# Performance work log

Measured on AMD Instinct MI355X. Metric: run time of the kernel, lower is better.

## Reference

```python
import jax, jax.numpy as jnp
import numpy as np

N_NODES = 20000; N_EDGES = 320000; B = 128; T = 200
EMB = 128; GH = 64; HEADS = 4; LH = 128; NSP = 64; TD = 4

def gat_conv(x, src, dst, W, att_src, att_dst, bias, heads, ch, concat):
    # PyG GATConv (eval mode, dropout off): per-edge attention + segment softmax over dst
    n = x.shape[0]
    h = (x @ W).reshape(n, heads, ch)                      # [N,H,C]
    a_s = (h * att_src[None]).sum(-1)                      # [N,H]
    a_d = (h * att_dst[None]).sum(-1)
    e = jax.nn.leaky_relu(a_s[src] + a_d[dst], 0.2)        # [E,H]
    e_max = jax.ops.segment_max(e, dst, num_segments=n)    # every node has a self-loop -> finite
    ex = jnp.exp(e - e_max[dst])
    denom = jax.ops.segment_sum(ex, dst, num_segments=n)
    alpha = ex / denom[dst]                                # [E,H]
    out = jax.ops.segment_sum(h[src] * alpha[:, :, None], dst, num_segments=n)  # [N,H,C]
    out = out.reshape(n, heads * ch) if concat else out.mean(axis=1)
    return out + bias

def lstm_dir(x, w_ih, w_hh, b):
    # single-direction LSTM, torch gate order (i, f, g, o)
    bsz = x.shape[0]
    def step(carry, xt):
        hprev, cprev = carry
        g = xt @ w_ih.T + hprev @ w_hh.T + b
        i, f, gg, o = jnp.split(g, 4, axis=-1)
        c = jax.nn.sigmoid(f) * cprev + jax.nn.sigmoid(i) * jnp.tanh(gg)
        hnew = jax.nn.sigmoid(o) * jnp.tanh(c)
        return (hnew, c), hnew
    init = (jnp.zeros((bsz, LH), x.dtype), jnp.zeros((bsz, LH), x.dtype))
    _, hs = jax.lax.scan(step, init, jnp.swapaxes(x, 0, 1))
    return jnp.swapaxes(hs, 0, 1)

def forward(x_coords, temporal_features, node_emb,
            gat1_W, gat1_att_src, gat1_att_dst, gat1_bias,
            gat2_W, gat2_att_src, gat2_att_dst, gat2_bias,
            w_ih_f, w_hh_f, b_f, w_ih_b, w_hh_b, b_b,
            attn_node_w, attn_node_b, attn_sp_w, attn_sp_b,
            fc_node_W, fc_node_b, fc_sp_W, fc_sp_b,
            edge_index, seq, lengths):
    n = x_coords.shape[0]
    node_features = jnp.concatenate([x_coords, node_emb, temporal_features], axis=1)  # [N,134]
    loops = jnp.arange(n)                                  # PyG GATConv add_self_loops=True
    src = jnp.concatenate([edge_index[0], loops])
    dst = jnp.concatenate([edge_index[1], loops])
    z = jax.nn.elu(gat_conv(node_features, src, dst, gat1_W, gat1_att_src, gat1_att_dst, gat1_bias, HEADS, GH, True))
    z = gat_conv(z, src, dst, gat2_W, gat2_att_src, gat2_att_dst, gat2_bias, 1, EMB, False)
    seq_emb = z[seq]                                       # [B,T,EMB]
    out_f = lstm_dir(seq_emb, w_ih_f, w_hh_f, b_f)
    # backward direction of packed BiLSTM: reverse each sequence within its true length
    rev_idx = jnp.clip(lengths[:, None] - 1 - jnp.arange(T)[None, :], 0, T - 1)
    x_rev = jnp.take_along_axis(seq_emb, rev_idx[:, :, None], axis=1)
    out_b = jnp.take_along_axis(lstm_dir(x_rev, w_ih_b, w_hh_b, b_b), rev_idx[:, :, None], axis=1)
    lstm_out = jnp.concatenate([out_f, out_b], axis=-1)    # [B,T,2*LH]
    mask = jnp.arange(T)[None, :] < lengths[:, None]
    def attnpool(w, bias):
        scores = jnp.where(mask, lstm_out @ w + bias, -jnp.inf)
        aw = jax.nn.softmax(scores, axis=1)
        return jnp.einsum('bt,bth->bh', aw, lstm_out)
    ctx_n = attnpool(attn_node_w, attn_node_b)
    ctx_s = attnpool(attn_sp_w, attn_sp_b)
    return (ctx_n @ fc_node_W + fc_node_b, ctx_s @ fc_sp_W + fc_sp_b)

def setup_inputs() -> dict:
    key = jax.random.key(0)
    ks = jax.random.split(key, 24)
    f = lambda i, shape, s=0.05: jax.random.normal(ks[i], shape, jnp.float32) * s
    return dict(
        x_coords=f(0, (N_NODES, 2), 1.0),
        temporal_features=f(1, (N_NODES, TD), 1.0),
        node_emb=f(2, (N_NODES, EMB)),
        gat1_W=f(3, (2 + EMB + TD, HEADS * GH)),
        gat1_att_src=f(4, (HEADS, GH)),
        gat1_att_dst=f(5, (HEADS, GH)),
        gat1_bias=jnp.zeros((HEADS * GH,), jnp.float32),
        gat2_W=f(6, (HEADS * GH, EMB)),
        gat2_att_src=f(7, (1, EMB)),
        gat2_att_dst=f(8, (1, EMB)),
        gat2_bias=jnp.zeros((EMB,), jnp.float32),
        w_ih_f=f(9, (4 * LH, EMB)), w_hh_f=f(10, (4 * LH, LH)), b_f=jnp.zeros((4 * LH,), jnp.float32),
        w_ih_b=f(11, (4 * LH, EMB)), w_hh_b=f(12, (4 * LH, LH)), b_b=jnp.zeros((4 * LH,), jnp.float32),
        attn_node_w=f(13, (2 * LH,)), attn_node_b=jnp.zeros((1,), jnp.float32),
        attn_sp_w=f(14, (2 * LH,)), attn_sp_b=jnp.zeros((1,), jnp.float32),
        fc_node_W=f(15, (2 * LH, N_NODES)), fc_node_b=jnp.zeros((N_NODES,), jnp.float32),
        fc_sp_W=f(16, (2 * LH, NSP)), fc_sp_b=jnp.zeros((NSP,), jnp.float32),
        edge_index=jax.random.randint(ks[17], (2, N_EDGES), 0, N_NODES),
        seq=jax.random.randint(ks[18], (B, T), 0, N_NODES),
        lengths=jax.random.randint(ks[19], (B,), 1, T + 1),
    )

def reference(x_coords, temporal_features, node_emb,
              gat1_W, gat1_att_src, gat1_att_dst, gat1_bias,
              gat2_W, gat2_att_src, gat2_att_dst, gat2_bias,
              w_ih_f, w_hh_f, b_f, w_ih_b, w_hh_b, b_b,
              attn_node_w, attn_node_b, attn_sp_w, attn_sp_b,
              fc_node_W, fc_node_b, fc_sp_W, fc_sp_b,
              edge_index, seq, lengths):
    return forward(x_coords, temporal_features, node_emb,
                   gat1_W, gat1_att_src, gat1_att_dst, gat1_bias,
                   gat2_W, gat2_att_src, gat2_att_dst, gat2_bias,
                   w_ih_f, w_hh_f, b_f, w_ih_b, w_hh_b, b_b,
                   attn_node_w, attn_node_b, attn_sp_w, attn_sp_b,
                   fc_node_W, fc_node_b, fc_sp_W, fc_sp_b,
                   edge_index, seq, lengths)
```

## Files before the change

kernel.cpp:

```cpp
#include <hip/hip_runtime.h>
#include <cstdint>
#include <cstddef>

#define N_NODES 20000
#define N_EDGES 320000
#define NE_TOT  (N_EDGES + N_NODES)
#define BB 128
#define TT 200
#define EMB 128
#define GH 64
#define HEADS 4
#define LH 128
#define NSP 64
#define KF 136

#define NB_COUNT  ((NE_TOT + 255) / 256)
#define NB_PREP1  (N_NODES + KF)
#define NB_PREP2  ((2 * 512 * 128 + 512 + 255) / 256)
#define NB_ROWMAP ((BB * TT + 255) / 256)

__global__ void k_prep_all(const int* __restrict__ ei, int* __restrict__ cnt,
                           const float* __restrict__ xc, const float* __restrict__ tf,
                           const float* __restrict__ ne, const float* __restrict__ W1,
                           float* __restrict__ nf, float* __restrict__ Wp,
                           const float* __restrict__ wf, const float* __restrict__ wb,
                           const float* __restrict__ bf, const float* __restrict__ bb,
                           float* __restrict__ WT, float* __restrict__ bcat,
                           const int* __restrict__ lengths, const int* __restrict__ seq,
                           int* __restrict__ rowsrc, int* __restrict__ rowdst,
                           int* __restrict__ loff)
{
    int blk = blockIdx.x;
    int tid = threadIdx.x;
    if (blk < NB_COUNT) {
        int e = blk * 256 + tid;
        if (e >= NE_TOT) return;
        int d = (e < N_EDGES) ? ei[N_EDGES + e] : (e - N_EDGES);
        atomicAdd(&cnt[d], 1);
    } else if (blk < NB_COUNT + NB_PREP1) {
        int b2 = blk - NB_COUNT;
        if (b2 < N_NODES) {
            int n = b2, j = tid;
            if (j >= KF) return;
            float v = 0.f;
            if (j < 2)        v = xc[n * 2 + j];
            else if (j < 130) v = ne[n * 128 + (j - 2)];
            else if (j < 134) v = tf[n * 4 + (j - 130)];
            nf[(size_t)n * KF + j] = v;
        } else {
            int k = b2 - N_NODES, n = tid;
            Wp[k * 256 + n] = (k < 134) ? W1[k * 256 + n] : 0.f;
        }
    } else if (blk < NB_COUNT + NB_PREP1 + NB_PREP2) {
        int idx = (blk - NB_COUNT - NB_PREP1) * 256 + tid;
        if (idx < 512 * 128) {
            int g = idx & 511, k = idx >> 9;
            WT[k * 1024 + g] = wf[g * 128 + k];
        } else if (idx < 2 * 512 * 128) {
            int j = idx - 512 * 128;
            int g = j & 511, k = j >> 9;
            WT[k * 1024 + 512 + g] = wb[g * 128 + k];
        } else if (idx < 2 * 512 * 128 + 512) {
            int t = idx - 2 * 512 * 128;
            bcat[t] = bf[t];
            bcat[512 + t] = bb[t];
        }
    } else {
        int idx = (blk - NB_COUNT - NB_PREP1 - NB_PREP2) * 256 + tid;
        if (idx >= BB * TT) return;
        int b = idx / TT, t = idx - b * TT;
        int base = 0;
        for (int i = 0; i < BB; i++) base += (i < b) ? lengths[i] : 0;
        if (idx == 0) {
            int tot = 0;
            for (int i = 0; i < BB; i++) tot += lengths[i];
            loff[BB] = tot;
        }
        if (t >= lengths[b]) return;
        int pos = base + t;
        rowsrc[pos] = seq[idx];
        rowdst[pos] = idx;
    }
}

__global__ __launch_bounds__(1024) void k_scan(const int* __restrict__ cnt,
                                               int* __restrict__ rs,
                                               int* __restrict__ cursor) {
    __shared__ int sd[1024];
    int tid = threadIdx.x;
    const int EPT = 20;
    int base = tid * EPT;
    int v[EPT];
    int s = 0;
#pragma unroll
    for (int i = 0; i < EPT; i++) {
        int idx = base + i;
        v[i] = (idx < N_NODES) ? cnt[idx] : 0;
        s += v[i];
    }
    int x = s;
    sd[tid] = x;
    __syncthreads();
    for (int off = 1; off < 1024; off <<= 1) {
        int t = (tid >= off) ? sd[tid - off] : 0;
        __syncthreads();
        x += t; sd[tid] = x;
        __syncthreads();
    }
    int run = x - s;
#pragma unroll
    for (int i = 0; i < EPT; i++) {
        int idx = base + i;
        if (idx < N_NODES) { rs[idx] = run; cursor[idx] = run; }
        run += v[i];
    }
    if (tid == 1023) rs[N_NODES] = x;
}

__global__ void k_scatter(const int* __restrict__ ei, int* __restrict__ cursor, int* __restrict__ csr) {
    int e = blockIdx.x * blockDim.x + threadIdx.x;
    if (e >= NE_TOT) return;
    int s, d;
    if (e < N_EDGES) { s = ei[e]; d = ei[N_EDGES + e]; }
    else             { s = d = e - N_EDGES; }
    int pos = atomicAdd(&cursor[d], 1);
    csr[pos] = s;
}

__global__ __launch_bounds__(256) void k_gemm_f32(
    const float* __restrict__ A, const float* __restrict__ B, float* __restrict__ C,
    int M, int N, int K, const int* __restrict__ gather, const float* __restrict__ bias,
    const float* __restrict__ asrc, const float* __restrict__ adst,
    float* __restrict__ a_s, float* __restrict__ a_d, int AC)
{
    __shared__ float As[8][68];
    __shared__ float Bs[8][68];
    int tid = threadIdx.x;
    int bm = blockIdx.y << 6, bn = blockIdx.x << 6;
    int tm = (tid >> 4) << 2, tn = (tid & 15) << 2;
    float acc[4][4] = {};
    for (int k0 = 0; k0 < K; k0 += 8) {
        if (tid < 128) {
            int m = tid >> 1, kq = (tid & 1) << 2;
            int gm = bm + m;
            float4 v = make_float4(0.f, 0.f, 0.f, 0.f);
            if (gm < M) {
                int row = gather ? gather[gm] : gm;
                v = *(const float4*)(A + (size_t)row * K + k0 + kq);
            }
            As[kq + 0][m] = v.x; As[kq + 1][m] = v.y;
            As[kq + 2][m] = v.z; As[kq + 3][m] = v.w;
        } else {
            int t2 = tid - 128;
            int kk = t2 >> 4, n4 = (t2 & 15) << 2;
            int gn = bn + n4;
            float4 v = make_float4(0.f, 0.f, 0.f, 0.f);
            const float* brow = B + (size_t)(k0 + kk) * N;
            if (gn + 3 < N) v = *(const float4*)(brow + gn);
            else {
                if (gn + 0 < N) v.x = brow[gn + 0];
                if (gn + 1 < N) v.y = brow[gn + 1];
                if (gn + 2 < N) v.z = brow[gn + 2];
                if (gn + 3 < N) v.w = brow[gn + 3];
            }
            *(float4*)(&Bs[kk][n4]) = v;
        }
        __syncthreads();
#pragma unroll
        for (int k = 0; k < 8; k++) {
            float4 av = *(const float4*)&As[k][tm];
            float4 bv = *(const float4*)&Bs[k][tn];
            acc[0][0] += av.x * bv.x; acc[0][1] += av.x * bv.y; acc[0][2] += av.x * bv.z; acc[0][3] += av.x * bv.w;
            acc[1][0] += av.y * bv.x; acc[1][1] += av.y * bv.y; acc[1][2] += av.y * bv.z; acc[1][3] += av.y * bv.w;
            acc[2][0] += av.z * bv.x; acc[2][1] += av.z * bv.y; acc[2][2] += av.z * bv.z; acc[2][3] += av.z * bv.w;
            acc[3][0] += av.w * bv.x; acc[3][1] += av.w * bv.y; acc[3][2] += av.w * bv.z; acc[3][3] += av.w * bv.w;
        }
        __syncthreads();
    }
#pragma unroll
    for (int i = 0; i < 4; i++) {
        int gm = bm + tm + i;
        if (gm >= M) continue;
#pragma unroll
        for (int j = 0; j < 4; j++) {
            int gn = bn + tn + j;
            if (gn >= N) continue;
            float r = acc[i][j];
            if (bias) r += bias[gn];
            C[(size_t)gm * N + gn] = r;
        }
    }
    if (asrc) {
        int H = N / AC;
        int h = bn / AC;
#pragma unroll
        for (int i = 0; i < 4; i++) {
            int gm = bm + tm + i;
            float ps = 0.f, pd = 0.f;
#pragma unroll
            for (int j = 0; j < 4; j++) {
                int gn = bn + tn + j;
                ps += acc[i][j] * asrc[gn];
                pd += acc[i][j] * adst[gn];
            }
            for (int off = 8; off >= 1; off >>= 1) {
                ps += __shfl_down(ps, off);
                pd += __shfl_down(pd, off);
            }
            if ((tid & 15) == 0 && gm < M) {
                atomicAdd(&a_s[gm * H + h], ps);
                atomicAdd(&a_d[gm * H + h], pd);
            }
        }
    }
}

__global__ __launch_bounds__(256) void k_gemm_f32_rs(
    const float* __restrict__ A, const float* __restrict__ B, float* __restrict__ C,
    const int* __restrict__ Mdev, int N, int K,
    const int* __restrict__ rowsrc, const int* __restrict__ rowdst,
    const float* __restrict__ bias)
{
    int M = Mdev[BB];
    int bm = blockIdx.y << 6, bn = blockIdx.x << 6;
    if (bm >= M) return;
    __shared__ float As[8][68];
    __shared__ float Bs[8][68];
    int tid = threadIdx.x;
    int tm = (tid >> 4) << 2, tn = (tid & 15) << 2;
    float acc[4][4] = {};
    for (int k0 = 0; k0 < K; k0 += 8) {
        if (tid < 128) {
            int m = tid >> 1, kq = (tid & 1) << 2;
            int gm = bm + m;
            float4 v = make_float4(0.f, 0.f, 0.f, 0.f);
            if (gm < M) {
                int row = rowsrc[gm];
                v = *(const float4*)(A + (size_t)row * K + k0 + kq);
            }
            As[kq + 0][m] = v.x; As[kq + 1][m] = v.y;
            As[kq + 2][m] = v.z; As[kq + 3][m] = v.w;
        } else {
            int t2 = tid - 128;
            int kk = t2 >> 4, n4 = (t2 & 15) << 2;
            int gn = bn + n4;
            const float* brow = B + (size_t)(k0 + kk) * N;
            *(float4*)(&Bs[kk][n4]) = *(const float4*)(brow + gn);
        }
        __syncthreads();
#pragma unroll
        for (int k = 0; k < 8; k++) {
            float4 av = *(const float4*)&As[k][tm];
            float4 bv = *(const float4*)&Bs[k][tn];
            acc[0][0] += av.x * bv.x; acc[0][1] += av.x * bv.y; acc[0][2] += av.x * bv.z; acc[0][3] += av.x * bv.w;
            acc[1][0] += av.y * bv.x; acc[1][1] += av.y * bv.y; acc[1][2] += av.y * bv.z; acc[1][3] += av.y * bv.w;
            acc[2][0] += av.z * bv.x; acc[2][1] += av.z * bv.y; acc[2][2] += av.z * bv.z; acc[2][3] += av.z * bv.w;
            acc[3][0] += av.w * bv.x; acc[3][1] += av.w * bv.y; acc[3][2] += av.w * bv.z; acc[3][3] += av.w * bv.w;
        }
        __syncthreads();
    }
#pragma unroll
    for (int i = 0; i < 4; i++) {
        int gm = bm + tm + i;
        if (gm >= M) continue;
        size_t crow = (size_t)rowdst[gm] * N;
#pragma unroll
        for (int j = 0; j < 4; j++) {
            int gn = bn + tn + j;
            float r = acc[i][j] + bias[gn];
            C[crow + gn] = r;
        }
    }
}

__global__ __launch_bounds__(256) void k_gemm_heads(
    const float* __restrict__ ctxn, const float* __restrict__ ctxs,
    const float* __restrict__ Wn, const float* __restrict__ bnod,
    const float* __restrict__ Wsp, const float* __restrict__ bsp,
    float* __restrict__ outn, float* __restrict__ outs)
{
    const float* A; const float* B; float* C; const float* bias; int N; int bn;
    if (blockIdx.x < 313) { A = ctxn; B = Wn;  C = outn; bias = bnod; N = N_NODES; bn = blockIdx.x << 6; }
    else                  { A = ctxs; B = Wsp; C = outs; bias = bsp;  N = NSP;     bn = 0; }
    const int M = BB, K = 2 * LH;
    __shared__ float As[8][68];
    __shared__ float Bs[8][68];
    int tid = threadIdx.x;
    int bm = blockIdx.y << 6;
    int tm = (tid >> 4) << 2, tn = (tid & 15) << 2;
    float acc[4][4] = {};
    for (int k0 = 0; k0 < K; k0 += 8) {
        if (tid < 128) {
            int m = tid >> 1, kq = (tid & 1) << 2;
            int gm = bm + m;
            float4 v = make_float4(0.f, 0.f, 0.f, 0.f);
            if (gm < M) v = *(const float4*)(A + (size_t)gm * K + k0 + kq);
            As[kq + 0][m] = v.x; As[kq + 1][m] = v.y;
            As[kq + 2][m] = v.z; As[kq + 3][m] = v.w;
        } else {
            int t2 = tid - 128;
            int kk = t2 >> 4, n4 = (t2 & 15) << 2;
            int gn = bn + n4;
            float4 v = make_float4(0.f, 0.f, 0.f, 0.f);
            const float* brow = B + (size_t)(k0 + kk) * N;
            if (gn + 3 < N) v = *(const float4*)(brow + gn);
            else {
                if (gn + 0 < N) v.x = brow[gn + 0];
                if (gn + 1 < N) v.y = brow[gn + 1];
                if (gn + 2 < N) v.z = brow[gn + 2];
                if (gn + 3 < N) v.w = brow[gn + 3];
            }
            *(float4*)(&Bs[kk][n4]) = v;
        }
        __syncthreads();
#pragma unroll
        for (int k = 0; k < 8; k++) {
            float4 av = *(const float4*)&As[k][tm];
            float4 bv = *(const float4*)&Bs[k][tn];
            acc[0][0] += av.x * bv.x; acc[0][1] += av.x * bv.y; acc[0][2] += av.x * bv.z; acc[0][3] += av.x * bv.w;
            acc[1][0] += av.y * bv.x; acc[1][1] += av.y * bv.y; acc[1][2] += av.y * bv.z; acc[1][3] += av.y * bv.w;
            acc[2][0] += av.z * bv.x; acc[2][1] += av.z * bv.y; acc[2][2] += av.z * bv.z; acc[2][3] += av.z * bv.w;
            acc[3][0] += av.w * bv.x; acc[3][1] += av.w * bv.y; acc[3][2] += av.w * bv.z; acc[3][3] += av.w * bv.w;
        }
        __syncthreads();
    }
#pragma unroll
    for (int i = 0; i < 4; i++) {
        int gm = bm + tm + i;
        if (gm >= M) continue;
#pragma unroll
        for (int j = 0; j < 4; j++) {
            int gn = bn + tn + j;
            if (gn >= N) continue;
            C[(size_t)gm * N + gn] = acc[i][j] + bias[gn];
        }
    }
}

template <int H, int C, bool DO_ELU>
__global__ void k_gat_aggregate(const float* __restrict__ hm, const float* __restrict__ a_s,
                                const float* __restrict__ a_d, const int* __restrict__ rs,
                                const int* __restrict__ csr, const float* __restrict__ bias,
                                float* __restrict__ out) {
    int d = blockIdx.x;
    int tid = threadIdx.x;
    int h = tid / C;
    int r0 = rs[d], r1 = rs[d + 1];
    float adv = a_d[d * H + h];
    float den = 0.f, acc = 0.f;
    for (int j = r0; j < r1; j++) {
        int s = csr[j];
        float e = a_s[s * H + h] + adv;
        e = (e > 0.f) ? e : 0.2f * e;
        float ex = __expf(e);
        den += ex;
        acc += ex * hm[(size_t)s * (H * C) + tid];
    }
    float r = acc / den + bias[tid];
    if (DO_ELU) r = (r > 0.f) ? r : expm1f(r);
    out[(size_t)d * (H * C) + tid] = r;
}

__device__ __forceinline__ float sigmf(float x) { return 1.f / (1.f + __expf(-x)); }
__device__ __forceinline__ float tanhfast(float x) {
    x = fminf(fmaxf(x, -20.f), 20.f);
    float e = __expf(2.f * x);
    return (e - 1.f) / (e + 1.f);
}

__global__ __launch_bounds__(512, 2) void k_lstm(
    const float* __restrict__ xgcat,
    const float* __restrict__ whh_f, const float* __restrict__ whh_b,
    const int* __restrict__ lengths, float* __restrict__ lstm_out)
{
    int b = blockIdx.x & 127;
    int dir = blockIdx.x >> 7;
    int tid = threadIdx.x;
    int u = tid & 127;
    int j = tid >> 7;
    const float* whh = dir ? whh_b : whh_f;
    const float* xg = xgcat + (dir << 9);
    int L = lengths[b];
    float4 w4[4][8];
#pragma unroll
    for (int m = 0; m < 4; m++) {
        const float4* wrow = (const float4*)(whh + (size_t)(m * LH + u) * LH + j * 32);
#pragma unroll
        for (int q = 0; q < 8; q++) w4[m][q] = wrow[q];
    }
    __shared__ float hbuf[LH];
    __shared__ float pbuf[4][4 * LH];
    if (tid < LH) hbuf[tid] = 0.f;
    float c = 0.f;
    float hv = 0.f;
    float x0 = 0.f, x1 = 0.f, x2 = 0.f, x3 = 0.f;
    if (j == 0) {
        int tx0 = dir ? (L - 1) : 0;
        const float* xrow = xg + ((size_t)(b * TT + tx0) << 10);
        x0 = xrow[u]; x1 = xrow[LH + u]; x2 = xrow[2 * LH + u]; x3 = xrow[3 * LH + u];
    }
    __syncthreads();
    for (int t = 0; t < L; t++) {
        if (j == 0 && t > 0) {
            int txp = dir ? (L - t) : (t - 1);
            lstm_out[((size_t)b * TT + txp) * (2 * LH) + dir * LH + u] = hv;
        }
        float x0n = 0.f, x1n = 0.f, x2n = 0.f, x3n = 0.f;
        if (j == 0 && t + 1 < L) {
            int tx1 = dir ? (L - 2 - t) : (t + 1);
            const float* xrow = xg + ((size_t)(b * TT + tx1) << 10);
            x0n = xrow[u]; x1n = xrow[LH + u]; x2n = xrow[2 * LH + u]; x3n = xrow[3 * LH + u];
        }
        const float4* hp = (const float4*)(hbuf + j * 32);
        float4 h[8];
#pragma unroll
        for (int q = 0; q < 8; q++) h[q] = hp[q];
        float a0 = x0, a1 = x1, a2 = x2, a3 = x3;
#pragma unroll
        for (int q = 0; q < 8; q++) {
            float4 hq = h[q];
            a0 += w4[0][q].x * hq.x + w4[0][q].y * hq.y + w4[0][q].z * hq.z + w4[0][q].w * hq.w;
            a1 += w4[1][q].x * hq.x + w4[1][q].y * hq.y + w4[1][q].z * hq.z + w4[1][q].w * hq.w;
            a2 += w4[2][q].x * hq.x + w4[2][q].y * hq.y + w4[2][q].z * hq.z + w4[2][q].w * hq.w;
            a3 += w4[3][q].x * hq.x + w4[3][q].y * hq.y + w4[3][q].z * hq.z + w4[3][q].w * hq.w;
        }
        pbuf[j][0 * LH + u] = a0;
        pbuf[j][1 * LH + u] = a1;
        pbuf[j][2 * LH + u] = a2;
        pbuf[j][3 * LH + u] = a3;
        asm volatile("s_waitcnt lgkmcnt(0)" ::: "memory");
        __builtin_amdgcn_sched_barrier(0);
        __builtin_amdgcn_s_barrier();
        if (tid < LH) {
            float gi = (pbuf[0][0 * LH + u] + pbuf[1][0 * LH + u]) + (pbuf[2][0 * LH + u] + pbuf[3][0 * LH + u]);
            float gf = (pbuf[0][1 * LH + u] + pbuf[1][1 * LH + u]) + (pbuf[2][1 * LH + u] + pbuf[3][1 * LH + u]);
            float gG = (pbuf[0][2 * LH + u] + pbuf[1][2 * LH + u]) + (pbuf[2][2 * LH + u] + pbuf[3][2 * LH + u]);
            float go = (pbuf[0][3 * LH + u] + pbuf[1][3 * LH + u]) + (pbuf[2][3 * LH + u] + pbuf[3][3 * LH + u]);
            float ig = sigmf(gi);
            float fg = sigmf(gf);
            float gg = tanhfast(gG);
            float og = sigmf(go);
            c = fg * c + ig * gg;
            hv = og * tanhfast(c);
            hbuf[u] = hv;
        }
        asm volatile("s_waitcnt lgkmcnt(0)" ::: "memory");
        __builtin_amdgcn_sched_barrier(0);
        __builtin_amdgcn_s_barrier();
        x0 = x0n; x1 = x1n; x2 = x2n; x3 = x3n;
    }
    if (j == 0) {
        int txp = dir ? 0 : (L - 1);
        lstm_out[((size_t)b * TT + txp) * (2 * LH) + dir * LH + u] = hv;
    }
}

__global__ __launch_bounds__(256) void k_attnpool(
    const float* __restrict__ lo, const int* __restrict__ lengths,
    const float* __restrict__ wn, const float* __restrict__ bn,
    const float* __restrict__ wsp, const float* __restrict__ bsp,
    float* __restrict__ ctxn, float* __restrict__ ctxs)
{
    int b = blockIdx.x;
    int tid = threadIdx.x;
    int L = lengths[b];
    __shared__ float sn[TT], ss[TT];
    __shared__ float red[256];
    int wv = tid >> 6, lane = tid & 63;
    for (int t = wv; t < L; t += 4) {
        const float* row = lo + ((size_t)b * TT + t) * (2 * LH);
        float pn = 0.f, ps = 0.f;
#pragma unroll
        for (int c0 = 0; c0 < 256; c0 += 64) {
            float v = row[c0 + lane];
            pn += v * wn[c0 + lane];
            ps += v * wsp[c0 + lane];
        }
#pragma unroll
        for (int off = 32; off > 0; off >>= 1) {
            pn += __shfl_down(pn, off);
            ps += __shfl_down(ps, off);
        }
        if (lane == 0) { sn[t] = pn + bn[0]; ss[t] = ps + bsp[0]; }
    }
    __syncthreads();
    float vn = (tid < L) ? sn[tid] : -1e30f;
    float vs = (tid < L) ? ss[tid] : -1e30f;
    red[tid] = vn; __syncthreads();
    for (int s = 128; s > 0; s >>= 1) { if (tid < s) red[tid] = fmaxf(red[tid], red[tid + s]); __syncthreads(); }
    float mn = red[0]; __syncthreads();
    red[tid] = vs; __syncthreads();
    for (int s = 128; s > 0; s >>= 1) { if (tid < s) red[tid] = fmaxf(red[tid], red[tid + s]); __syncthreads(); }
    float ms = red[0]; __syncthreads();
    float en = (tid < L) ? __expf(vn - mn) : 0.f;
    float es = (tid < L) ? __expf(vs - ms) : 0.f;
    red[tid] = en; __syncthreads();
    for (int s = 128; s > 0; s >>= 1) { if (tid < s) red[tid] += red[tid + s]; __syncthreads(); }
    float dn = red[0]; __syncthreads();
    red[tid] = es; __syncthreads();
    for (int s = 128; s > 0; s >>= 1) { if (tid < s) red[tid] += red[tid + s]; __syncthreads(); }
    float dsum = red[0]; __syncthreads();
    if (tid < L) { sn[tid] = en / dn; ss[tid] = es / dsum; }
    __syncthreads();
    float an = 0.f, asv = 0.f;
    for (int t = 0; t < L; t++) {
        float v = lo[((size_t)b * TT + t) * (2 * LH) + tid];
        an += sn[t] * v;
        asv += ss[t] * v;
    }
    ctxn[b * (2 * LH) + tid] = an;
    ctxs[b * (2 * LH) + tid] = asv;
}

extern "C" void kernel_launch(void* const* d_in, const int* in_sizes, int n_in,
                              void* d_out, int out_size, void* d_ws, size_t ws_size,
                              hipStream_t stream) {
    (void)in_sizes; (void)n_in; (void)out_size; (void)ws_size;
    const float* x_coords = (const float*)d_in[0];
    const float* temporal = (const float*)d_in[1];
    const float* node_emb = (const float*)d_in[2];
    const float* gat1_W   = (const float*)d_in[3];
    const float* gat1_as  = (const float*)d_in[4];
    const float* gat1_ad  = (const float*)d_in[5];
    const float* gat1_b   = (const float*)d_in[6];
    const float* gat2_W   = (const float*)d_in[7];
    const float* gat2_as  = (const float*)d_in[8];
    const float* gat2_ad  = (const float*)d_in[9];
    const float* gat2_b   = (const float*)d_in[10];
    const float* w_ih_f   = (const float*)d_in[11];
    const float* w_hh_f   = (const float*)d_in[12];
    const float* b_f      = (const float*)d_in[13];
    const float* w_ih_b   = (const float*)d_in[14];
    const float* w_hh_b   = (const float*)d_in[15];
    const float* b_b      = (const float*)d_in[16];
    const float* attn_n_w = (const float*)d_in[17];
    const float* attn_n_b = (const float*)d_in[18];
    const float* attn_s_w = (const float*)d_in[19];
    const float* attn_s_b = (const float*)d_in[20];
    const float* fc_n_W   = (const float*)d_in[21];
    const float* fc_n_b   = (const float*)d_in[22];
    const float* fc_s_W   = (const float*)d_in[23];
    const float* fc_s_b   = (const float*)d_in[24];
    const int*   edge_idx = (const int*)d_in[25];
    const int*   seq      = (const int*)d_in[26];
    const int*   lengths  = (const int*)d_in[27];

    char* ws = (char*)d_ws;
    size_t off = 0;
    auto alloc = [&](size_t bytes) -> char* {
        char* p = ws + off;
        off += (bytes + 255) & ~(size_t)255;
        return p;
    };
    int*   cnt      = (int*)alloc((size_t)N_NODES * 4);
    float* as1      = (float*)alloc((size_t)N_NODES * 4 * 4);
    float* ad1      = (float*)alloc((size_t)N_NODES * 4 * 4);
    float* as2      = (float*)alloc((size_t)N_NODES * 4);
    float* ad2      = (float*)alloc((size_t)N_NODES * 4);
    size_t zero_end = off;
    int*   rowstart = (int*)alloc((size_t)(N_NODES + 1) * 4);
    int*   cursor   = (int*)alloc((size_t)N_NODES * 4);
    int*   csr      = (int*)alloc((size_t)NE_TOT * 4);
    float* z2       = (float*)alloc((size_t)N_NODES * EMB * 4);
    float* lstm_o   = (float*)alloc((size_t)BB * TT * 2 * LH * 4);
    float* ctxn     = (float*)alloc((size_t)BB * 2 * LH * 4);
    float* ctxs     = (float*)alloc((size_t)BB * 2 * LH * 4);
    float* wTcat    = (float*)alloc((size_t)128 * 1024 * 4);
    float* bcat     = (float*)alloc((size_t)1024 * 4);
    int*   loff     = (int*)alloc((size_t)(BB + 1) * 4);
    int*   rowsrc   = (int*)alloc((size_t)BB * TT * 4);
    int*   rowdst   = (int*)alloc((size_t)BB * TT * 4);
    float* nf  = (float*)(ws + off);
    float* w1p = nf + (size_t)N_NODES * KF;
    float* h1  = w1p + (size_t)KF * 256;
    float* z1  = h1 + (size_t)N_NODES * 256;
    float* h2  = z1 + (size_t)N_NODES * 256;
    float* xgcat = (float*)(ws + off);

    hipMemsetAsync(cnt, 0, zero_end, stream);
    k_prep_all<<<NB_COUNT + NB_PREP1 + NB_PREP2 + NB_ROWMAP, 256, 0, stream>>>(
        edge_idx, cnt, x_coords, temporal, node_emb, gat1_W, nf, w1p,
        w_ih_f, w_ih_b, b_f, b_b, wTcat, bcat, lengths, seq, rowsrc, rowdst, loff);
    k_scan<<<1, 1024, 0, stream>>>(cnt, rowstart, cursor);
    k_scatter<<<(NE_TOT + 255) / 256, 256, 0, stream>>>(edge_idx, cursor, csr);
    {
        dim3 g(4, (N_NODES + 63) / 64);
        k_gemm_f32<<<g, 256, 0, stream>>>(nf, w1p, h1, N_NODES, 256, KF, nullptr, nullptr,
                                          gat1_as, gat1_ad, as1, ad1, GH);
    }
    k_gat_aggregate<HEADS, GH, true><<<N_NODES, 256, 0, stream>>>(h1, as1, ad1, rowstart, csr, gat1_b, z1);
    {
        dim3 g(2, (N_NODES + 63) / 64);
        k_gemm_f32<<<g, 256, 0, stream>>>(z1, gat2_W, h2, N_NODES, 128, 256, nullptr, nullptr,
                                          gat2_as, gat2_ad, as2, ad2, EMB);
    }
    k_gat_aggregate<1, EMB, false><<<N_NODES, 128, 0, stream>>>(h2, as2, ad2, rowstart, csr, gat2_b, z2);
    {
        dim3 g(1024 / 64, (BB * TT + 63) / 64);
        k_gemm_f32_rs<<<g, 256, 0, stream>>>(z2, wTcat, xgcat, loff, 1024, 128, rowsrc, rowdst, bcat);
    }
    k_lstm<<<256, 512, 0, stream>>>(xgcat, w_hh_f, w_hh_b, lengths, lstm_o);
    k_attnpool<<<BB, 256, 0, stream>>>(lstm_o, lengths, attn_n_w, attn_n_b, attn_s_w, attn_s_b, ctxn, ctxs);
    float* out_node = (float*)d_out;
    float* out_sp   = out_node + (size_t)BB * N_NODES;
    {
        dim3 g(314, 2);
        k_gemm_heads<<<g, 256, 0, stream>>>(ctxn, ctxs, fc_n_W, fc_n_b, fc_s_W, fc_s_b, out_node, out_sp);
    }
}
```

Before: 687.2 us.

## Rewrite FP32 GEMMs as single-wave 8x8 register tiles with double-buffered LDS

All four dense GEMM kernels (both GAT projections, the LSTM input projection and the output heads) move from 256-thread blocks computing 4x4 per thread to 64-thread single-wavefront blocks computing 8x8 per thread. The next K-slice is prefetched into registers and written to a second LDS buffer, and __syncthreads is replaced by an lgkmcnt wait plus a scheduling barrier. Output stores become float4. This raises arithmetic intensity per LDS read and removes block barriers, but each CU now holds fewer waves, which lowers occupancy and latency hiding on the smaller grids.

```diff
diff --git a/kernel.cpp b/kernel.cpp
--- a/kernel.cpp
+++ b/kernel.cpp
@@ -18,6 +18,11 @@
 #define NB_PREP1  (N_NODES + KF)
 #define NB_PREP2  ((2 * 512 * 128 + 512 + 255) / 256)
 #define NB_ROWMAP ((BB * TT + 255) / 256)
+
+#define LDS_FENCE() do { \
+    asm volatile("s_waitcnt lgkmcnt(0)" ::: "memory"); \
+    __builtin_amdgcn_sched_barrier(0); \
+} while (0)
 
 __global__ void k_prep_all(const int* __restrict__ ei, int* __restrict__ cnt,
                            const float* __restrict__ xc, const float* __restrict__ tf,
@@ -127,95 +132,90 @@
     csr[pos] = s;
 }
 
-__global__ __launch_bounds__(256) void k_gemm_f32(
+__global__ __launch_bounds__(64) void k_wgemm_attn(
     const float* __restrict__ A, const float* __restrict__ B, float* __restrict__ C,
-    int M, int N, int K, const int* __restrict__ gather, const float* __restrict__ bias,
+    int M, int N, int K,
     const float* __restrict__ asrc, const float* __restrict__ adst,
     float* __restrict__ a_s, float* __restrict__ a_d, int AC)
 {
-    __shared__ float As[8][68];
-    __shared__ float Bs[8][68];
+    __shared__ float As[2][8][68];
+    __shared__ float Bs[2][8][68];
     int tid = threadIdx.x;
     int bm = blockIdx.y << 6, bn = blockIdx.x << 6;
-    int tm = (tid >> 4) << 2, tn = (tid & 15) << 2;
-    float acc[4][4] = {};
-    for (int k0 = 0; k0 < K; k0 += 8) {
-        if (tid < 128) {
-            int m = tid >> 1, kq = (tid & 1) << 2;
-            int gm = bm + m;
-            float4 v = make_float4(0.f, 0.f, 0.f, 0.f);
-            if (gm < M) {
-                int row = gather ? gather[gm] : gm;
-                v = *(const float4*)(A + (size_t)row * K + k0 + kq);
-            }
-            As[kq + 0][m] = v.x; As[kq + 1][m] = v.y;
-            As[kq + 2][m] = v.z; As[kq + 3][m] = v.w;
-        } else {
-            int t2 = tid - 128;
-            int kk = t2 >> 4, n4 = (t2 & 15) << 2;
-            int gn = bn + n4;
-            float4 v = make_float4(0.f, 0.f, 0.f, 0.f);
-            const float* brow = B + (size_t)(k0 + kk) * N;
-            if (gn + 3 < N) v = *(const float4*)(brow + gn);
-            else {
-                if (gn + 0 < N) v.x = brow[gn + 0];
-                if (gn + 1 < N) v.y = brow[gn + 1];
-                if (gn + 2 < N) v.z = brow[gn + 2];
-                if (gn + 3 < N) v.w = brow[gn + 3];
-            }
-            *(float4*)(&Bs[kk][n4]) = v;
-        }
-        __syncthreads();
+    int r8 = tid >> 3, c8 = tid & 7;
+    int arow = (bm + tid < M) ? (bm + tid) : -1;
+    int bkk = tid >> 3;
+    int gnb = bn + (c8 << 3);
+    float acc[8][8] = {};
+    float4 va0, va1, vb0, vb1;
+    auto loadAB = [&](int k0) {
+        va0 = va1 = make_float4(0.f, 0.f, 0.f, 0.f);
+        if (arow >= 0) {
+            const float* ap = A + (size_t)arow * K + k0;
+            va0 = *(const float4*)ap; va1 = *(const float4*)(ap + 4);
+        }
+        const float* bp = B + (size_t)(k0 + bkk) * N + gnb;
+        vb0 = *(const float4*)bp; vb1 = *(const float4*)(bp + 4);
+    };
+    auto writeAB = [&](int buf) {
+        As[buf][0][tid] = va0.x; As[buf][1][tid] = va0.y;
+        As[buf][2][tid] = va0.z; As[buf][3][tid] = va0.w;
+        As[buf][4][tid] = va1.x; As[buf][5][tid] = va1.y;
+        As[buf][6][tid] = va1.z; As[buf][7][tid] = va1.w;
+        *(float4*)&Bs[buf][bkk][c8 << 3] = vb0;
+        *(float4*)&Bs[buf][bkk][(c8 << 3) + 4] = vb1;
+    };
+    loadAB(0); writeAB(0);
+    int nk = K >> 3, cur = 0;
+    for (int ki = 0; ki < nk; ki++) {
+        bool more = (ki + 1 < nk);
+        if (more) loadAB((ki + 1) << 3);
+        LDS_FENCE();
 #pragma unroll
         for (int k = 0; k < 8; k++) {
-            float4 av = *(const float4*)&As[k][tm];
-            float4 bv = *(const float4*)&Bs[k][tn];
-            acc[0][0] += av.x * bv.x; acc[0][1] += av.x * bv.y; acc[0][2] += av.x * bv.z; acc[0][3] += av.x * bv.w;
-            acc[1][0] += av.y * bv.x; acc[1][1] += av.y * bv.y; acc[1][2] += av.y * bv.z; acc[1][3] += av.y * bv.w;
-            acc[2][0] += av.z * bv.x; acc[2][1] += av.z * bv.y; acc[2][2] += av.z * bv.z; acc[2][3] += av.z * bv.w;
-            acc[3][0] += av.w * bv.x; acc[3][1] += av.w * bv.y; acc[3][2] += av.w * bv.z; acc[3][3] += av.w * bv.w;
-        }
-        __syncthreads();
-    }
-#pragma unroll
-    for (int i = 0; i < 4; i++) {
-        int gm = bm + tm + i;
+            const float* ar = &As[cur][k][r8 << 3];
+            const float* br = &Bs[cur][k][c8 << 3];
+            float4 a0 = *(const float4*)ar, a1 = *(const float4*)(ar + 4);
+            float4 b0 = *(const float4*)br, b1 = *(const float4*)(br + 4);
+            float av[8] = {a0.x, a0.y, a0.z, a0.w, a1.x, a1.y, a1.z, a1.w};
+            float bv[8] = {b0.x, b0.y, b0.z, b0.w, b1.x, b1.y, b1.z, b1.w};
+#pragma unroll
+            for (int i = 0; i < 8; i++)
+#pragma unroll
+                for (int j = 0; j < 8; j++) acc[i][j] += av[i] * bv[j];
+        }
+        if (more) writeAB(cur ^ 1);
+        cur ^= 1;
+    }
+#pragma unroll
+    for (int i = 0; i < 8; i++) {
+        int gm = bm + (r8 << 3) + i;
         if (gm >= M) continue;
-#pragma unroll
-        for (int j = 0; j < 4; j++) {
-            int gn = bn + tn + j;
-            if (gn >= N) continue;
-            float r = acc[i][j];
-            if (bias) r += bias[gn];
-            C[(size_t)gm * N + gn] = r;
-        }
-    }
-    if (asrc) {
-        int H = N / AC;
-        int h = bn / AC;
-#pragma unroll
-        for (int i = 0; i < 4; i++) {
-            int gm = bm + tm + i;
-            float ps = 0.f, pd = 0.f;
-#pragma unroll
-            for (int j = 0; j < 4; j++) {
-                int gn = bn + tn + j;
-                ps += acc[i][j] * asrc[gn];
-                pd += acc[i][j] * adst[gn];
-            }
-            for (int off = 8; off >= 1; off >>= 1) {
-                ps += __shfl_down(ps, off);
-                pd += __shfl_down(pd, off);
-            }
-            if ((tid & 15) == 0 && gm < M) {
-                atomicAdd(&a_s[gm * H + h], ps);
-                atomicAdd(&a_d[gm * H + h], pd);
-            }
-        }
-    }
-}
-
-__global__ __launch_bounds__(256) void k_gemm_f32_rs(
+        float* crow = C + (size_t)gm * N + gnb;
+        *(float4*)crow = make_float4(acc[i][0], acc[i][1], acc[i][2], acc[i][3]);
+        *(float4*)(crow + 4) = make_float4(acc[i][4], acc[i][5], acc[i][6], acc[i][7]);
+    }
+    int H = N / AC, h = bn / AC;
+#pragma unroll
+    for (int i = 0; i < 8; i++) {
+        float ps = 0.f, pd = 0.f;
+#pragma unroll
+        for (int j = 0; j < 8; j++) {
+            int gn = gnb + j;
+            ps += acc[i][j] * asrc[gn];
+            pd += acc[i][j] * adst[gn];
+        }
+        ps += __shfl_xor(ps, 1); ps += __shfl_xor(ps, 2); ps += __shfl_xor(ps, 4);
+        pd += __shfl_xor(pd, 1); pd += __shfl_xor(pd, 2); pd += __shfl_xor(pd, 4);
+        int gm = bm + (r8 << 3) + i;
+        if (c8 == 0 && gm < M) {
+            atomicAdd(&a_s[gm * H + h], ps);
+            atomicAdd(&a_d[gm * H + h], pd);
+        }
+    }
+}
+
+__global__ __launch_bounds__(64) void k_wgemm_rs(
     const float* __restrict__ A, const float* __restrict__ B, float* __restrict__ C,
     const int* __restrict__ Mdev, int N, int K,
     const int* __restrict__ rowsrc, const int* __restrict__ rowdst,
@@ -224,56 +224,67 @@
     int M = Mdev[BB];
     int bm = blockIdx.y << 6, bn = blockIdx.x << 6;
     if (bm >= M) return;
-    __shared__ float As[8][68];
-    __shared__ float Bs[8][68];
-    int tid = threadIdx.x;
-    int tm = (tid >> 4) << 2, tn = (tid & 15) << 2;
-    float acc[4][4] = {};
-    for (int k0 = 0; k0 < K; k0 += 8) {
-        if (tid < 128) {
-            int m = tid >> 1, kq = (tid & 1) << 2;
-            int gm = bm + m;
-            float4 v = make_float4(0.f, 0.f, 0.f, 0.f);
-            if (gm < M) {
-                int row = rowsrc[gm];
-                v = *(const float4*)(A + (size_t)row * K + k0 + kq);
-            }
-            As[kq + 0][m] = v.x; As[kq + 1][m] = v.y;
-            As[kq + 2][m] = v.z; As[kq + 3][m] = v.w;
-        } else {
-            int t2 = tid - 128;
-            int kk = t2 >> 4, n4 = (t2 & 15) << 2;
-            int gn = bn + n4;
-            const float* brow = B + (size_t)(k0 + kk) * N;
-            *(float4*)(&Bs[kk][n4]) = *(const float4*)(brow + gn);
-        }
-        __syncthreads();
+    __shared__ float As[2][8][68];
+    __shared__ float Bs[2][8][68];
+    int tid = threadIdx.x;
+    int r8 = tid >> 3, c8 = tid & 7;
+    int arow = (bm + tid < M) ? rowsrc[bm + tid] : -1;
+    int bkk = tid >> 3;
+    int gnb = bn + (c8 << 3);
+    float acc[8][8] = {};
+    float4 va0, va1, vb0, vb1;
+    auto loadAB = [&](int k0) {
+        va0 = va1 = make_float4(0.f, 0.f, 0.f, 0.f);
+        if (arow >= 0) {
+            const float* ap = A + (size_t)arow * K + k0;
+            va0 = *(const float4*)ap; va1 = *(const float4*)(ap + 4);
+        }
+        const float* bp = B + (size_t)(k0 + bkk) * N + gnb;
+        vb0 = *(const float4*)bp; vb1 = *(const float4*)(bp + 4);
+    };
+    auto writeAB = [&](int buf) {
+        As[buf][0][tid] = va0.x; As[buf][1][tid] = va0.y;
+        As[buf][2][tid] = va0.z; As[buf][3][tid] = va0.w;
+        As[buf][4][tid] = va1.x; As[buf][5][tid] = va1.y;
+        As[buf][6][tid] = va1.z; As[buf][7][tid] = va1.w;
+        *(float4*)&Bs[buf][bkk][c8 << 3] = vb0;
+        *(float4*)&Bs[buf][bkk][(c8 << 3) + 4] = vb1;
+    };
+    loadAB(0); writeAB(0);
+    int nk = K >> 3, cur = 0;
+    for (int ki = 0; ki < nk; ki++) {
+        bool more = (ki + 1 < nk);
+        if (more) loadAB((ki + 1) << 3);
+        LDS_FENCE();
 #pragma unroll
         for (int k = 0; k < 8; k++) {
-            float4 av = *(const float4*)&As[k][tm];
-            float4 bv = *(const float4*)&Bs[k][tn];
-            acc[0][0] += av.x * bv.x; acc[0][1] += av.x * bv.y; acc[0][2] += av.x * bv.z; acc[0][3] += av.x * bv.w;
-            acc[1][0] += av.y * bv.x; acc[1][1] += av.y * bv.y; acc[1][2] += av.y * bv.z; acc[1][3] += av.y * bv.w;
-            acc[2][0] += av.z * bv.x; acc[2][1] += av.z * bv.y; acc[2][2] += av.z * bv.z; acc[2][3] += av.z * bv.w;
-            acc[3][0] += av.w * bv.x; acc[3][1] += av.w * bv.y; acc[3][2] += av.w * bv.z; acc[3][3] += av.w * bv.w;
-        }
-        __syncthreads();
-    }
-#pragma unroll
-    for (int i = 0; i < 4; i++) {
-        int gm = bm + tm + i;
+            const float* ar = &As[cur][k][r8 << 3];
+            const float* br = &Bs[cur][k][c8 << 3];
+            float4 a0 = *(const float4*)ar, a1 = *(const float4*)(ar + 4);
+            float4 b0 = *(const float4*)br, b1 = *(const float4*)(br + 4);
+            float av[8] = {a0.x, a0.y, a0.z, a0.w, a1.x, a1.y, a1.z, a1.w};
+            float bv[8] = {b0.x, b0.y, b0.z, b0.w, b1.x, b1.y, b1.z, b1.w};
+#pragma unroll
+            for (int i = 0; i < 8; i++)
+#pragma unroll
+                for (int j = 0; j < 8; j++) acc[i][j] += av[i] * bv[j];
+        }
+        if (more) writeAB(cur ^ 1);
+        cur ^= 1;
+    }
+#pragma unroll
+    for (int i = 0; i < 8; i++) {
+        int gm = bm + (r8 << 3) + i;
         if (gm >= M) continue;
-        size_t crow = (size_t)rowdst[gm] * N;
-#pragma unroll
-        for (int j = 0; j < 4; j++) {
-            int gn = bn + tn + j;
-            float r = acc[i][j] + bias[gn];
-            C[crow + gn] = r;
-        }
-    }
-}
-
-__global__ __launch_bounds__(256) void k_gemm_heads(
+        float* crow = C + (size_t)rowdst[gm] * N + gnb;
+        *(float4*)crow = make_float4(acc[i][0] + bias[gnb + 0], acc[i][1] + bias[gnb + 1],
+                                     acc[i][2] + bias[gnb + 2], acc[i][3] + bias[gnb + 3]);
+        *(float4*)(crow + 4) = make_float4(acc[i][4] + bias[gnb + 4], acc[i][5] + bias[gnb + 5],
+                                           acc[i][6] + bias[gnb + 6], acc[i][7] + bias[gnb + 7]);
+    }
+}
+
+__global__ __launch_bounds__(64) void k_wheads(
     const float* __restrict__ ctxn, const float* __restrict__ ctxs,
     const float* __restrict__ Wn, const float* __restrict__ bnod,
     const float* __restrict__ Wsp, const float* __restrict__ bsp,
@@ -283,57 +294,67 @@
     if (blockIdx.x < 313) { A = ctxn; B = Wn;  C = outn; bias = bnod; N = N_NODES; bn = blockIdx.x << 6; }
     else                  { A = ctxs; B = Wsp; C = outs; bias = bsp;  N = NSP;     bn = 0; }
     const int M = BB, K = 2 * LH;
-    __shared__ float As[8][68];
-    __shared__ float Bs[8][68];
+    __shared__ float As[2][8][68];
+    __shared__ float Bs[2][8][68];
     int tid = threadIdx.x;
     int bm = blockIdx.y << 6;
-    int tm = (tid >> 4) << 2, tn = (tid & 15) << 2;
-    float acc[4][4] = {};
-    for (int k0 = 0; k0 < K; k0 += 8) {
-        if (tid < 128) {
-            int m = tid >> 1, kq = (tid & 1) << 2;
-            int gm = bm + m;
-            float4 v = make_float4(0.f, 0.f, 0.f, 0.f);
-            if (gm < M) v = *(const float4*)(A + (size_t)gm * K + k0 + kq);
-            As[kq + 0][m] = v.x; As[kq + 1][m] = v.y;
-            As[kq + 2][m] = v.z; As[kq + 3][m] = v.w;
-        } else {
-            int t2 = tid - 128;
-            int kk = t2 >> 4, n4 = (t2 & 15) << 2;
-            int gn = bn + n4;
-            float4 v = make_float4(0.f, 0.f, 0.f, 0.f);
-            const float* brow = B + (size_t)(k0 + kk) * N;
-            if (gn + 3 < N) v = *(const float4*)(brow + gn);
-            else {
-                if (gn + 0 < N) v.x = brow[gn + 0];
-                if (gn + 1 < N) v.y = brow[gn + 1];
-                if (gn + 2 < N) v.z = brow[gn + 2];
-                if (gn + 3 < N) v.w = brow[gn + 3];
-            }
-            *(float4*)(&Bs[kk][n4]) = v;
-        }
-        __syncthreads();
+    int r8 = tid >> 3, c8 = tid & 7;
+    int arow = (bm + tid < M) ? (bm + tid) : -1;
+    int bkk = tid >> 3;
+    int gnb = bn + (c8 << 3);
+    float acc[8][8] = {};
+    float4 va0, va1, vb0, vb1;
+    auto loadAB = [&](int k0) {
+        va0 = va1 = vb0 = vb1 = make_float4(0.f, 0.f, 0.f, 0.f);
+        if (arow >= 0) {
+            const float* ap = A + (size_t)arow * K + k0;
+            va0 = *(const float4*)ap; va1 = *(const float4*)(ap + 4);
+        }
+        const float* bp = B + (size_t)(k0 + bkk) * N + gnb;
+        if (gnb < N)     vb0 = *(const float4*)bp;
+        if (gnb + 4 < N) vb1 = *(const float4*)(bp + 4);
+    };
+    auto writeAB = [&](int buf) {
+        As[buf][0][tid] = va0.x; As[buf][1][tid] = va0.y;
+        As[buf][2][tid] = va0.z; As[buf][3][tid] = va0.w;
+        As[buf][4][tid] = va1.x; As[buf][5][tid] = va1.y;
+        As[buf][6][tid] = va1.z; As[buf][7][tid] = va1.w;
+        *(float4*)&Bs[buf][bkk][c8 << 3] = vb0;
+        *(float4*)&Bs[buf][bkk][(c8 << 3) + 4] = vb1;
+    };
+    loadAB(0); writeAB(0);
+    int nk = K >> 3, cur = 0;
+    for (int ki = 0; ki < nk; ki++) {
+        bool more = (ki + 1 < nk);
+        if (more) loadAB((ki + 1) << 3);
+        LDS_FENCE();
 #pragma unroll
         for (int k = 0; k < 8; k++) {
-            float4 av = *(const float4*)&As[k][tm];
-            float4 bv = *(const float4*)&Bs[k][tn];
-            acc[0][0] += av.x * bv.x; acc[0][1] += av.x * bv.y; acc[0][2] += av.x * bv.z; acc[0][3] += av.x * bv.w;
-            acc[1][0] += av.y * bv.x; acc[1][1] += av.y * bv.y; acc[1][2] += av.y * bv.z; acc[1][3] += av.y * bv.w;
-            acc[2][0] += av.z * bv.x; acc[2][1] += av.z * bv.y; acc[2][2] += av.z * bv.z; acc[2][3] += av.z * bv.w;
-            acc[3][0] += av.w * bv.x; acc[3][1] += av.w * bv.y; acc[3][2] += av.w * bv.z; acc[3][3] += av.w * bv.w;
-        }
-        __syncthreads();
-    }
-#pragma unroll
-    for (int i = 0; i < 4; i++) {
-        int gm = bm + tm + i;
+            const float* ar = &As[cur][k][r8 << 3];
+            const float* br = &Bs[cur][k][c8 << 3];
+            float4 a0 = *(const float4*)ar, a1 = *(const float4*)(ar + 4);
+            float4 b0 = *(const float4*)br, b1 = *(const float4*)(br + 4);
+            float av[8] = {a0.x, a0.y, a0.z, a0.w, a1.x, a1.y, a1.z, a1.w};
+            float bv[8] = {b0.x, b0.y, b0.z, b0.w, b1.x, b1.y, b1.z, b1.w};
+#pragma unroll
+            for (int i = 0; i < 8; i++)
+#pragma unroll
+                for (int j = 0; j < 8; j++) acc[i][j] += av[i] * bv[j];
+        }
+        if (more) writeAB(cur ^ 1);
+        cur ^= 1;
+    }
+#pragma unroll
+    for (int i = 0; i < 8; i++) {
+        int gm = bm + (r8 << 3) + i;
         if (gm >= M) continue;
-#pragma unroll
-        for (int j = 0; j < 4; j++) {
-            int gn = bn + tn + j;
-            if (gn >= N) continue;
-            C[(size_t)gm * N + gn] = acc[i][j] + bias[gn];
-        }
+        float* crow = C + (size_t)gm * N + gnb;
+        if (gnb < N)
+            *(float4*)crow = make_float4(acc[i][0] + bias[gnb + 0], acc[i][1] + bias[gnb + 1],
+                                         acc[i][2] + bias[gnb + 2], acc[i][3] + bias[gnb + 3]);
+        if (gnb + 4 < N)
+            *(float4*)(crow + 4) = make_float4(acc[i][4] + bias[gnb + 4], acc[i][5] + bias[gnb + 5],
+                                               acc[i][6] + bias[gnb + 6], acc[i][7] + bias[gnb + 7]);
     }
 }
 
@@ -585,19 +606,19 @@
     k_scatter<<<(NE_TOT + 255) / 256, 256, 0, stream>>>(edge_idx, cursor, csr);
     {
         dim3 g(4, (N_NODES + 63) / 64);
-        k_gemm_f32<<<g, 256, 0, stream>>>(nf, w1p, h1, N_NODES, 256, KF, nullptr, nullptr,
-                                          gat1_as, gat1_ad, as1, ad1, GH);
+        k_wgemm_attn<<<g, 64, 0, stream>>>(nf, w1p, h1, N_NODES, 256, KF,
+                                           gat1_as, gat1_ad, as1, ad1, GH);
     }
     k_gat_aggregate<HEADS, GH, true><<<N_NODES, 256, 0, stream>>>(h1, as1, ad1, rowstart, csr, gat1_b, z1);
     {
         dim3 g(2, (N_NODES + 63) / 64);
-        k_gemm_f32<<<g, 256, 0, stream>>>(z1, gat2_W, h2, N_NODES, 128, 256, nullptr, nullptr,
-                                          gat2_as, gat2_ad, as2, ad2, EMB);
+        k_wgemm_attn<<<g, 64, 0, stream>>>(z1, gat2_W, h2, N_NODES, 128, 256,
+                                           gat2_as, gat2_ad, as2, ad2, EMB);
     }
     k_gat_aggregate<1, EMB, false><<<N_NODES, 128, 0, stream>>>(h2, as2, ad2, rowstart, csr, gat2_b, z2);
     {
         dim3 g(1024 / 64, (BB * TT + 63) / 64);
-        k_gemm_f32_rs<<<g, 256, 0, stream>>>(z2, wTcat, xgcat, loff, 1024, 128, rowsrc, rowdst, bcat);
+        k_wgemm_rs<<<g, 64, 0, stream>>>(z2, wTcat, xgcat, loff, 1024, 128, rowsrc, rowdst, bcat);
     }
     k_lstm<<<256, 512, 0, stream>>>(xgcat, w_hh_f, w_hh_b, lengths, lstm_o);
     k_attnpool<<<BB, 256, 0, stream>>>(lstm_o, lengths, attn_n_w, attn_n_b, attn_s_w, attn_s_b, ctxn, ctxs);
@@ -605,6 +626,6 @@
     float* out_sp   = out_node + (size_t)BB * N_NODES;
     {
         dim3 g(314, 2);
-        k_gemm_heads<<<g, 256, 0, stream>>>(ctxn, ctxs, fc_n_W, fc_n_b, fc_s_W, fc_s_b, out_node, out_sp);
-    }
-}
+        k_wheads<<<g, 64, 0, stream>>>(ctxn, ctxs, fc_n_W, fc_n_b, fc_s_W, fc_s_b, out_node, out_sp);
+    }
+}
```

New measurement: 711.0 us. +3.5%, slower.
